# Optimization experiments

Hardware: AMD Instinct MI355X
Metric: run time of the kernel (lower is better)

Reference implementation:

```python
import jax, jax.numpy as jnp
import numpy as np

B = 64          # batch
C = 80          # num_classes
IN_CH = 300     # word-embedding channel
J = 8192        # JOINT_EMB_SIZE (linear_intermediate)
S = 8           # pooling_stride
OUT = J // S    # out_in_tmp = 1024


def setup_inputs() -> dict:
    key = jax.random.key(0)
    ks = jax.random.split(key, 8)
    w = lambda k, sh: jax.random.normal(k, sh, jnp.float32) * 0.02
    return {
        "feature": jax.random.normal(ks[0], (B, 2048, 14, 14), jnp.float32),
        "inp": jax.random.normal(ks[1], (1, C, IN_CH), jnp.float32),
        "A": jax.random.uniform(ks[2], (C, C), jnp.float32),  # positive co-occurrence adjacency
        "W_gc1": w(ks[3], (IN_CH, 1024)),
        "W_gc2": w(ks[4], (1024, 2048)),
        "W_img": w(ks[5], (J, 2048)),
        "b_img": jnp.zeros((J,), jnp.float32),
        "W_cls": w(ks[6], (J, 2048)),
        "b_cls": jnp.zeros((J,), jnp.float32),
        "W_ml": w(ks[7], (C, C * OUT)),
        "b_ml": jnp.zeros((C,), jnp.float32),
    }


def reference(feature, inp, A, W_gc1, W_gc2, W_img, b_img, W_cls, b_cls, W_ml, b_ml):
    # backbone output -> MaxPool2d(14,14) over a 14x14 map == global spatial max
    feat = feature.max(axis=(2, 3))                       # [B, 2048]

    # gen_adj(A).detach(): D = diag(rowsum(A)^-0.5); adj = D @ A.T @ D
    dinv = jnp.sum(A, axis=1) ** -0.5                     # [C]
    adj = jax.lax.stop_gradient(A.T * dinv[:, None] * dinv[None, :])  # [C, C]

    # two GCN layers on label embeddings
    x = adj @ (inp[0] @ W_gc1)                            # [C, 1024]
    x = jax.nn.leaky_relu(x, 0.2)
    x = adj @ (x @ W_gc2)                                 # [C, 2048]

    # MFB bilinear fusion (vectorized form of the nested batch/class loops;
    # dropout is identity in eval mode)
    img = feat @ W_img.T + b_img                          # [B, J]
    cls = x @ W_cls.T + b_cls                             # [C, J]
    # sum-pool over the stride axis of the elementwise product:
    # iq[b,c,o] = sum_s img[b,o*S+s] * cls[c,o*S+s]
    pooled = jnp.einsum('bos,cos->bco',
                        img.reshape(B, OUT, S),
                        cls.reshape(C, OUT, S))           # [B, C, OUT]
    # torch.cat order over class columns -> c-major flatten, then ML_fc_layer
    out = pooled.reshape(B, C * OUT) @ W_ml.T + b_ml      # [B, C]
    return out
```

## Files before the change

kernel.cpp:

```cpp
#include <hip/hip_runtime.h>
#include <hip/hip_bf16.h>
#include <cstdint>
#include <cstddef>

typedef float  f32x4  __attribute__((ext_vector_type(4)));
typedef __bf16 bf16x8 __attribute__((ext_vector_type(8)));
typedef unsigned short u16x8 __attribute__((ext_vector_type(8)));

__device__ __forceinline__ unsigned short f2bf(float f) {
    unsigned u = __float_as_uint(f);
    u += 0x7FFFu + ((u >> 16) & 1u);
    return (unsigned short)(u >> 16);
}


constexpr size_t OFF_FEATB = 0;
constexpr size_t OFF_ADJ   = 262144;
constexpr size_t OFF_Y0    = 287744;
constexpr size_t OFF_X1    = 615424;
constexpr size_t OFF_X2B   = 943104;
constexpr size_t OFF_WG2T  = 1106944;
constexpr size_t OFF_XB    = 9495552;
constexpr size_t OFF_IMG   = 9823232;
constexpr size_t OFF_CLS   = 11920384;
constexpr size_t OFF_G     = 14541824;


__device__ __forceinline__ void maxpool_role(int bid, const float* __restrict__ feature,
                                             unsigned short* __restrict__ featb) {
    int wave = threadIdx.x >> 6, lane = threadIdx.x & 63;
    int r = lane >> 4, q = lane & 15;
    #pragma unroll
    for (int it = 0; it < 4; ++it) {
        int row = bid * 128 + it * 32 + wave * 4 + r;
        const float4* p = (const float4*)(feature + (size_t)row * 196);
        float4 a = p[q], b = p[q + 16], c = p[q + 32];
        float m = fmaxf(fmaxf(fmaxf(a.x, a.y), fmaxf(a.z, a.w)),
                 fmaxf(fmaxf(fmaxf(b.x, b.y), fmaxf(b.z, b.w)),
                       fmaxf(fmaxf(c.x, c.y), fmaxf(c.z, c.w))));
        if (q == 0) {
            float4 d = p[48];
            m = fmaxf(m, fmaxf(fmaxf(d.x, d.y), fmaxf(d.z, d.w)));
        }
        #pragma unroll
        for (int off = 1; off < 16; off <<= 1) m = fmaxf(m, __shfl_xor(m, off));
        if (q == 0) featb[row] = f2bf(m);
    }
}

__device__ __forceinline__ void transpose_role(int idx, const float* __restrict__ in,
                                               float* __restrict__ out, float* t ) {
    int c0 = (idx & 31) * 64, r0 = (idx >> 5) * 64;
    int tx = threadIdx.x & 63, ty = threadIdx.x >> 6;
    #pragma unroll
    for (int i = 0; i < 64; i += 8)
        t[(ty + i) * 65 + tx] = in[(size_t)(r0 + ty + i) * 2048 + c0 + tx];
    __syncthreads();
    #pragma unroll
    for (int i = 0; i < 64; i += 8)
        out[(size_t)(c0 + ty + i) * 1024 + r0 + tx] = t[tx * 65 + (ty + i)];
}

__device__ __forceinline__ void y0_role(int idx, const float* __restrict__ inp,
                                        const float* __restrict__ W1, float* __restrict__ y0) {
    int c = idx >> 1;
    int j = (idx & 1) * 512 + threadIdx.x;
    const float* xr = inp + c * 300;
    float acc = 0.f;
    #pragma unroll 4
    for (int k = 0; k < 300; k++) acc = fmaf(xr[k], W1[k * 1024 + j], acc);
    y0[c * 1024 + j] = acc;
}

__device__ __forceinline__ void adj_role(const float* __restrict__ A, float* __restrict__ adjp,
                                         float* dinv ) {
    int t = threadIdx.x;
    if (t < 80) {
        float s = 0.f;
        for (int j = 0; j < 80; j++) s += A[t * 80 + j];
        dinv[t] = 1.0f / sqrtf(s);
    }
    __syncthreads();
    for (int i = t; i < 6400; i += 512) {
        int r = i / 80, cc = i % 80;
        adjp[i] = A[cc * 80 + r] * dinv[r] * dinv[cc];
    }
}

__device__ __forceinline__ void adjmul_role(int idx, const float* __restrict__ adjp,
                                            const float* __restrict__ xin,
                                            float* __restrict__ outf,
                                            unsigned short* __restrict__ outb, int leaky) {
    int c = idx >> 1;
    int j = (idx & 1) * 512 + threadIdx.x;
    const float* ar = adjp + c * 80;
    float acc = 0.f;
    #pragma unroll 4
    for (int k = 0; k < 80; k++) acc = fmaf(ar[k], xin[k * 1024 + j], acc);
    if (leaky && acc < 0.f) acc *= 0.2f;
    if (outf) outf[c * 1024 + j] = acc;
    if (outb) outb[c * 1024 + j] = f2bf(acc);
}

template <int MF>
__device__ __forceinline__ void gemm_block(int bx, const unsigned short* __restrict__ X,
                                           const float* __restrict__ W,
                                           const float* __restrict__ bias,
                                           float* __restrict__ outf,
                                           unsigned short* __restrict__ outb,
                                           int N, int K, float (*red)[64][21]) {
    int tid = threadIdx.x;
    int wave = tid >> 6, lane = tid & 63;
    int nf = wave & 1, ks = wave >> 1;
    int n = bx * 32 + nf * 16 + (lane & 15);
    int rowa = lane & 15;
    int koff = (lane >> 4) * 8;
    int Kc = K >> 2;
    int k0 = ks * Kc;

    f32x4 acc[MF];
    #pragma unroll
    for (int i = 0; i < MF; i++) acc[i] = (f32x4)(0.f);

    const float* wrow = W + (size_t)n * K;

    #pragma unroll 2
    for (int k = k0; k < k0 + Kc; k += 32) {
        float4 w0 = *(const float4*)(wrow + k + koff);
        float4 w1 = *(const float4*)(wrow + k + koff + 4);
        u16x8 bu;
        bu[0] = f2bf(w0.x); bu[1] = f2bf(w0.y); bu[2] = f2bf(w0.z); bu[3] = f2bf(w0.w);
        bu[4] = f2bf(w1.x); bu[5] = f2bf(w1.y); bu[6] = f2bf(w1.z); bu[7] = f2bf(w1.w);
        bf16x8 bf = __builtin_bit_cast(bf16x8, bu);
        #pragma unroll
        for (int mf = 0; mf < MF; mf++) {
            u16x8 au = *(const u16x8*)(X + (size_t)(mf * 16 + rowa) * K + k + koff);
            acc[mf] = __builtin_amdgcn_mfma_f32_16x16x32_bf16(
                __builtin_bit_cast(bf16x8, au), bf, acc[mf], 0, 0, 0);
        }
    }

    #pragma unroll
    for (int mf = 0; mf < MF; mf++)
        #pragma unroll
        for (int i = 0; i < 4; i++)
            red[wave][lane][mf * 4 + i] = acc[mf][i];
    __syncthreads();

    int lane2 = tid & 63, sg = (tid >> 6) & 3, nf2 = tid >> 8;
    int n2 = bx * 32 + nf2 * 16 + (lane2 & 15);
    float b = bias ? bias[n2] : 0.f;
    #pragma unroll
    for (int mf = 0; mf < MF; mf++) {
        int slot = mf * 4 + sg;
        float s = red[0 + nf2][lane2][slot] + red[2 + nf2][lane2][slot]
                + red[4 + nf2][lane2][slot] + red[6 + nf2][lane2][slot] + b;
        int row = mf * 16 + (lane2 >> 4) * 4 + sg;
        size_t o = (size_t)row * N + n2;
        if (outf) outf[o] = s;
        if (outb) outb[o] = f2bf(s);
    }
}


__global__ __launch_bounds__(512) void k1(const float* __restrict__ feature,
                                          unsigned short* __restrict__ featb,
                                          const float* __restrict__ inp,
                                          const float* __restrict__ W1,
                                          float* __restrict__ y0,
                                          const float* __restrict__ A,
                                          float* __restrict__ adjp,
                                          const float* __restrict__ Wg2,
                                          float* __restrict__ wg2t) {
    __shared__ float lds[64 * 65];
    int b = blockIdx.x;
    if (b < 1024)       maxpool_role(b, feature, featb);
    else if (b < 1536)  transpose_role(b - 1024, Wg2, wg2t, lds);
    else if (b < 1696)  y0_role(b - 1536, inp, W1, y0);
    else                adj_role(A, adjp, lds);
}

__global__ __launch_bounds__(512) void k2(const float* __restrict__ adjp,
                                          const float* __restrict__ y0,
                                          float* __restrict__ x1,
                                          const unsigned short* __restrict__ featb,
                                          const float* __restrict__ W_img,
                                          const float* __restrict__ b_img,
                                          float* __restrict__ img) {
    __shared__ float red[8][64][21];
    int b = blockIdx.x;
    if (b < 160) adjmul_role(b, adjp, y0, x1, nullptr, 1);
    else         gemm_block<4>(b - 160, featb, W_img, b_img, img, nullptr, 8192, 2048, red);
}

__global__ __launch_bounds__(512) void k3(const float* __restrict__ adjp,
                                          const float* __restrict__ x1,
                                          unsigned short* __restrict__ x2b) {
    adjmul_role(blockIdx.x, adjp, x1, nullptr, x2b, 0);
}

__global__ __launch_bounds__(512) void k4(const unsigned short* __restrict__ x2b,
                                          const float* __restrict__ wg2t,
                                          unsigned short* __restrict__ xb) {
    __shared__ float red[8][64][21];
    gemm_block<5>(blockIdx.x, x2b, wg2t, nullptr, nullptr, xb, 2048, 1024, red);
}

__global__ __launch_bounds__(512) void k5(const unsigned short* __restrict__ xb,
                                          const float* __restrict__ W_cls,
                                          const float* __restrict__ b_cls,
                                          float* __restrict__ cls) {
    __shared__ float red[8][64][21];
    gemm_block<5>(blockIdx.x, xb, W_cls, b_cls, cls, nullptr, 8192, 2048, red);
}

__global__ __launch_bounds__(256) void g_kernel(const float* __restrict__ cls,
                                                const float* __restrict__ W_ml,
                                                float* __restrict__ G) {
    __shared__ float wml[16][80][16];
    int c2b = blockIdx.y * 16;
    int o0  = blockIdx.x * 16;
    int j0  = o0 * 8;
    for (int idx = threadIdx.x; idx < 16 * 80 * 16; idx += 256) {
        int ol = idx & 15, c = (idx >> 4) % 80, c2 = idx / 1280;
        wml[c2][c][ol] = W_ml[(size_t)(c2b + c2) * 81920 + c * 1024 + o0 + ol];
    }
    __syncthreads();
    int jl  = threadIdx.x & 127;
    int c2l = (threadIdx.x >> 7) * 8;
    int ol  = jl >> 3;
    float acc[8] = {0.f, 0.f, 0.f, 0.f, 0.f, 0.f, 0.f, 0.f};
    for (int c = 0; c < 80; c++) {
        float cv = cls[(size_t)c * 8192 + j0 + jl];
        #pragma unroll
        for (int i = 0; i < 8; i++) acc[i] = fmaf(cv, wml[c2l + i][c][ol], acc[i]);
    }
    #pragma unroll
    for (int i = 0; i < 8; i++) G[(size_t)(c2b + c2l + i) * 8192 + j0 + jl] = acc[i];
}

__global__ __launch_bounds__(512) void k7(const float* __restrict__ img,
                                          const float* __restrict__ G,
                                          const float* __restrict__ b_ml,
                                          float* __restrict__ out) {
    __shared__ float sm[8][32];
    int btile = blockIdx.x, cg = blockIdx.y;
    int kc = threadIdx.x >> 6, lane = threadIdx.x & 63;
    float acc[4][8];
    #pragma unroll
    for (int q = 0; q < 4; q++)
        #pragma unroll
        for (int i = 0; i < 8; i++) acc[q][i] = 0.f;

    #pragma unroll
    for (int step = 0; step < 4; step++) {
        int k = kc * 1024 + step * 256 + lane * 4;
        float4 gv[8];
        #pragma unroll
        for (int i = 0; i < 8; i++) gv[i] = *(const float4*)(G + (size_t)(cg * 8 + i) * 8192 + k);
        #pragma unroll
        for (int q = 0; q < 4; q++) {
            float4 iv = *(const float4*)(img + (size_t)(btile * 4 + q) * 8192 + k);
            #pragma unroll
            for (int i = 0; i < 8; i++) {
                acc[q][i] = fmaf(iv.x, gv[i].x, acc[q][i]);
                acc[q][i] = fmaf(iv.y, gv[i].y, acc[q][i]);
                acc[q][i] = fmaf(iv.z, gv[i].z, acc[q][i]);
                acc[q][i] = fmaf(iv.w, gv[i].w, acc[q][i]);
            }
        }
    }
    #pragma unroll
    for (int q = 0; q < 4; q++)
        #pragma unroll
        for (int i = 0; i < 8; i++) {
            float v = acc[q][i];
            #pragma unroll
            for (int off = 32; off; off >>= 1) v += __shfl_xor(v, off);
            if (lane == 0) sm[kc][q * 8 + i] = v;
        }
    __syncthreads();
    if (threadIdx.x < 32) {
        int i = threadIdx.x & 7;
        float s = b_ml[cg * 8 + i];
        #pragma unroll
        for (int kk = 0; kk < 8; kk++) s += sm[kk][threadIdx.x];
        int q = threadIdx.x >> 3;
        out[(size_t)(btile * 4 + q) * 80 + cg * 8 + i] = s;
    }
}

extern "C" void kernel_launch(void* const* d_in, const int* in_sizes, int n_in,
                              void* d_out, int out_size, void* d_ws, size_t ws_size,
                              hipStream_t stream) {
    (void)in_sizes; (void)n_in; (void)out_size; (void)ws_size;
    const float* feature = (const float*)d_in[0];
    const float* inp     = (const float*)d_in[1];
    const float* A       = (const float*)d_in[2];
    const float* W_gc1   = (const float*)d_in[3];
    const float* W_gc2   = (const float*)d_in[4];
    const float* W_img   = (const float*)d_in[5];
    const float* b_img   = (const float*)d_in[6];
    const float* W_cls   = (const float*)d_in[7];
    const float* b_cls   = (const float*)d_in[8];
    const float* W_ml    = (const float*)d_in[9];
    const float* b_ml    = (const float*)d_in[10];
    float* out = (float*)d_out;
    char*  ws  = (char*)d_ws;

    unsigned short* featb = (unsigned short*)(ws + OFF_FEATB);
    float* adjp = (float*)(ws + OFF_ADJ);
    float* y0   = (float*)(ws + OFF_Y0);
    float* x1   = (float*)(ws + OFF_X1);
    unsigned short* x2b = (unsigned short*)(ws + OFF_X2B);
    float* wg2t = (float*)(ws + OFF_WG2T);
    unsigned short* xb  = (unsigned short*)(ws + OFF_XB);
    float* img  = (float*)(ws + OFF_IMG);
    float* cls  = (float*)(ws + OFF_CLS);
    float* G    = (float*)(ws + OFF_G);

    k1<<<1697, 512, 0, stream>>>(feature, featb, inp, W_gc1, y0, A, adjp, W_gc2, wg2t);
    k2<<<416,  512, 0, stream>>>(adjp, y0, x1, featb, W_img, b_img, img);
    k3<<<160,  512, 0, stream>>>(adjp, x1, x2b);
    k4<<<64,   512, 0, stream>>>(x2b, wg2t, xb);
    k5<<<256,  512, 0, stream>>>(xb, W_cls, b_cls, cls);
    g_kernel<<<dim3(64, 5), 256, 0, stream>>>(cls, W_ml, G);
    k7<<<dim3(16, 10), 512, 0, stream>>>(img, G, b_ml, out);
}
```

Baseline: 155.8 us.

## Spread maxpool across GCN stages, fuse img GEMM with G kernel, vectorize skinny matmuls

Splits the feature max-pool into four chunks and co-schedules them with the latency-bound GCN kernels (y0, the two adjacency multiplies, and the W_gc2 GEMM). This fills idle compute units during those small stages. The image GEMM moves out of the second kernel and is fused with the G (cls×W_ml) computation in one launch. The skinny matmuls now use float4 loads with a 4-way K split reduced through LDS. The cost is more launch-time role branching and larger shared memory per block in the fused kernel.

```diff
diff --git a/kernel.cpp b/kernel.cpp
--- a/kernel.cpp
+++ b/kernel.cpp
@@ -26,13 +26,14 @@
 constexpr size_t OFF_G     = 14541824;
 
 
-__device__ __forceinline__ void maxpool_role(int bid, const float* __restrict__ feature,
+__device__ __forceinline__ void maxpool_role(int base_row, int bid,
+                                             const float* __restrict__ feature,
                                              unsigned short* __restrict__ featb) {
     int wave = threadIdx.x >> 6, lane = threadIdx.x & 63;
     int r = lane >> 4, q = lane & 15;
     #pragma unroll
     for (int it = 0; it < 4; ++it) {
-        int row = bid * 128 + it * 32 + wave * 4 + r;
+        int row = base_row + bid * 128 + it * 32 + wave * 4 + r;
         const float4* p = (const float4*)(feature + (size_t)row * 196);
         float4 a = p[q], b = p[q + 16], c = p[q + 32];
         float m = fmaxf(fmaxf(fmaxf(a.x, a.y), fmaxf(a.z, a.w)),
@@ -48,6 +49,52 @@
     }
 }
 
+template <int KS>
+__device__ __forceinline__ void skinny_role(int idx, const float* __restrict__ X,
+                                            const float* __restrict__ W,
+                                            float* __restrict__ outf,
+                                            unsigned short* __restrict__ outb,
+                                            int leaky, float4* red ) {
+    int c = idx >> 1, jh = idx & 1;
+    int t = threadIdx.x;
+    int jq = t & 127, ks = t >> 7;
+    int j = jh * 512 + jq * 4;
+    const float* xr = X + c * 4 * KS + ks * KS;
+    const float* wp = W + (size_t)(ks * KS) * 1024 + j;
+    float4 acc = {0.f, 0.f, 0.f, 0.f};
+    #pragma unroll 5
+    for (int k = 0; k < KS; k++) {
+        float a = xr[k];
+        float4 w = *(const float4*)(wp + (size_t)k * 1024);
+        acc.x = fmaf(a, w.x, acc.x);
+        acc.y = fmaf(a, w.y, acc.y);
+        acc.z = fmaf(a, w.z, acc.z);
+        acc.w = fmaf(a, w.w, acc.w);
+    }
+    red[ks * 128 + jq] = acc;
+    __syncthreads();
+    if (ks == 0) {
+        float4 s0 = red[jq], s1 = red[128 + jq], s2 = red[256 + jq], s3 = red[384 + jq];
+        float4 s;
+        s.x = s0.x + s1.x + s2.x + s3.x;
+        s.y = s0.y + s1.y + s2.y + s3.y;
+        s.z = s0.z + s1.z + s2.z + s3.z;
+        s.w = s0.w + s1.w + s2.w + s3.w;
+        if (leaky) {
+            if (s.x < 0.f) s.x *= 0.2f;
+            if (s.y < 0.f) s.y *= 0.2f;
+            if (s.z < 0.f) s.z *= 0.2f;
+            if (s.w < 0.f) s.w *= 0.2f;
+        }
+        size_t o = (size_t)c * 1024 + j;
+        if (outf) *(float4*)(outf + o) = s;
+        if (outb) {
+            unsigned short b4[4] = {f2bf(s.x), f2bf(s.y), f2bf(s.z), f2bf(s.w)};
+            *(uint64_t*)(outb + o) = *(const uint64_t*)b4;
+        }
+    }
+}
+
 __device__ __forceinline__ void transpose_role(int idx, const float* __restrict__ in,
                                                float* __restrict__ out, float* t ) {
     int c0 = (idx & 31) * 64, r0 = (idx >> 5) * 64;
@@ -61,45 +108,24 @@
         out[(size_t)(c0 + ty + i) * 1024 + r0 + tx] = t[tx * 65 + (ty + i)];
 }
 
-__device__ __forceinline__ void y0_role(int idx, const float* __restrict__ inp,
-                                        const float* __restrict__ W1, float* __restrict__ y0) {
-    int c = idx >> 1;
-    int j = (idx & 1) * 512 + threadIdx.x;
-    const float* xr = inp + c * 300;
-    float acc = 0.f;
-    #pragma unroll 4
-    for (int k = 0; k < 300; k++) acc = fmaf(xr[k], W1[k * 1024 + j], acc);
-    y0[c * 1024 + j] = acc;
-}
-
 __device__ __forceinline__ void adj_role(const float* __restrict__ A, float* __restrict__ adjp,
                                          float* dinv ) {
     int t = threadIdx.x;
     if (t < 80) {
-        float s = 0.f;
-        for (int j = 0; j < 80; j++) s += A[t * 80 + j];
-        dinv[t] = 1.0f / sqrtf(s);
+        const float4* ar = (const float4*)(A + t * 80);
+        float4 s4 = {0.f, 0.f, 0.f, 0.f};
+        #pragma unroll
+        for (int j = 0; j < 20; j++) {
+            float4 v = ar[j];
+            s4.x += v.x; s4.y += v.y; s4.z += v.z; s4.w += v.w;
+        }
+        dinv[t] = 1.0f / sqrtf(s4.x + s4.y + s4.z + s4.w);
     }
     __syncthreads();
     for (int i = t; i < 6400; i += 512) {
         int r = i / 80, cc = i % 80;
         adjp[i] = A[cc * 80 + r] * dinv[r] * dinv[cc];
     }
-}
-
-__device__ __forceinline__ void adjmul_role(int idx, const float* __restrict__ adjp,
-                                            const float* __restrict__ xin,
-                                            float* __restrict__ outf,
-                                            unsigned short* __restrict__ outb, int leaky) {
-    int c = idx >> 1;
-    int j = (idx & 1) * 512 + threadIdx.x;
-    const float* ar = adjp + c * 80;
-    float acc = 0.f;
-    #pragma unroll 4
-    for (int k = 0; k < 80; k++) acc = fmaf(ar[k], xin[k * 1024 + j], acc);
-    if (leaky && acc < 0.f) acc *= 0.2f;
-    if (outf) outf[c * 1024 + j] = acc;
-    if (outb) outb[c * 1024 + j] = f2bf(acc);
 }
 
 template <int MF>
@@ -163,86 +189,105 @@
 }
 
 
-__global__ __launch_bounds__(512) void k1(const float* __restrict__ feature,
-                                          unsigned short* __restrict__ featb,
-                                          const float* __restrict__ inp,
-                                          const float* __restrict__ W1,
-                                          float* __restrict__ y0,
-                                          const float* __restrict__ A,
-                                          float* __restrict__ adjp,
-                                          const float* __restrict__ Wg2,
-                                          float* __restrict__ wg2t) {
-    __shared__ float lds[64 * 65];
-    int b = blockIdx.x;
-    if (b < 1024)       maxpool_role(b, feature, featb);
-    else if (b < 1536)  transpose_role(b - 1024, Wg2, wg2t, lds);
-    else if (b < 1696)  y0_role(b - 1536, inp, W1, y0);
-    else                adj_role(A, adjp, lds);
-}
-
-__global__ __launch_bounds__(512) void k2(const float* __restrict__ adjp,
-                                          const float* __restrict__ y0,
-                                          float* __restrict__ x1,
-                                          const unsigned short* __restrict__ featb,
-                                          const float* __restrict__ W_img,
-                                          const float* __restrict__ b_img,
-                                          float* __restrict__ img) {
-    __shared__ float red[8][64][21];
-    int b = blockIdx.x;
-    if (b < 160) adjmul_role(b, adjp, y0, x1, nullptr, 1);
-    else         gemm_block<4>(b - 160, featb, W_img, b_img, img, nullptr, 8192, 2048, red);
-}
-
-__global__ __launch_bounds__(512) void k3(const float* __restrict__ adjp,
-                                          const float* __restrict__ x1,
-                                          unsigned short* __restrict__ x2b) {
-    adjmul_role(blockIdx.x, adjp, x1, nullptr, x2b, 0);
-}
-
-__global__ __launch_bounds__(512) void k4(const unsigned short* __restrict__ x2b,
-                                          const float* __restrict__ wg2t,
-                                          unsigned short* __restrict__ xb) {
-    __shared__ float red[8][64][21];
-    gemm_block<5>(blockIdx.x, x2b, wg2t, nullptr, nullptr, xb, 2048, 1024, red);
-}
-
-__global__ __launch_bounds__(512) void k5(const unsigned short* __restrict__ xb,
-                                          const float* __restrict__ W_cls,
-                                          const float* __restrict__ b_cls,
-                                          float* __restrict__ cls) {
-    __shared__ float red[8][64][21];
+__global__ __launch_bounds__(512, 4) void kA(const float* __restrict__ inp,
+                                             const float* __restrict__ W1,
+                                             float* __restrict__ y0,
+                                             const float* __restrict__ A,
+                                             float* __restrict__ adjp,
+                                             const float* __restrict__ Wg2,
+                                             float* __restrict__ wg2t,
+                                             const float* __restrict__ feature,
+                                             unsigned short* __restrict__ featb) {
+    __shared__ __align__(16) float lds[64 * 65];
+    int b = blockIdx.x;
+    if (b < 160)       skinny_role<75>(b, inp, W1, y0, nullptr, 0, (float4*)lds);
+    else if (b < 161)  adj_role(A, adjp, lds);
+    else if (b < 673)  transpose_role(b - 161, Wg2, wg2t, lds);
+    else               maxpool_role(0, b - 673, feature, featb);
+}
+
+__global__ __launch_bounds__(512, 4) void kB(const float* __restrict__ adjp,
+                                             const float* __restrict__ y0,
+                                             float* __restrict__ x1,
+                                             const float* __restrict__ feature,
+                                             unsigned short* __restrict__ featb) {
+    __shared__ __align__(16) float4 red[512];
+    int b = blockIdx.x;
+    if (b < 160) skinny_role<20>(b, adjp, y0, x1, nullptr, 1, red);
+    else         maxpool_role(32768, b - 160, feature, featb);
+}
+
+__global__ __launch_bounds__(512, 4) void kC(const float* __restrict__ adjp,
+                                             const float* __restrict__ x1,
+                                             unsigned short* __restrict__ x2b,
+                                             const float* __restrict__ feature,
+                                             unsigned short* __restrict__ featb) {
+    __shared__ __align__(16) float4 red[512];
+    int b = blockIdx.x;
+    if (b < 160) skinny_role<20>(b, adjp, x1, nullptr, x2b, 0, red);
+    else         maxpool_role(65536, b - 160, feature, featb);
+}
+
+__global__ __launch_bounds__(512, 4) void kD(const unsigned short* __restrict__ x2b,
+                                             const float* __restrict__ wg2t,
+                                             unsigned short* __restrict__ xb,
+                                             const float* __restrict__ feature,
+                                             unsigned short* __restrict__ featb) {
+    __shared__ __align__(16) float red[8][64][21];
+    int b = blockIdx.x;
+    if (b < 64) gemm_block<5>(b, x2b, wg2t, nullptr, nullptr, xb, 2048, 1024, red);
+    else        maxpool_role(98304, b - 64, feature, featb);
+}
+
+__global__ __launch_bounds__(512, 4) void kE(const unsigned short* __restrict__ xb,
+                                             const float* __restrict__ W_cls,
+                                             const float* __restrict__ b_cls,
+                                             float* __restrict__ cls) {
+    __shared__ __align__(16) float red[8][64][21];
     gemm_block<5>(blockIdx.x, xb, W_cls, b_cls, cls, nullptr, 8192, 2048, red);
 }
 
-__global__ __launch_bounds__(256) void g_kernel(const float* __restrict__ cls,
-                                                const float* __restrict__ W_ml,
-                                                float* __restrict__ G) {
-    __shared__ float wml[16][80][16];
-    int c2b = blockIdx.y * 16;
-    int o0  = blockIdx.x * 16;
-    int j0  = o0 * 8;
-    for (int idx = threadIdx.x; idx < 16 * 80 * 16; idx += 256) {
-        int ol = idx & 15, c = (idx >> 4) % 80, c2 = idx / 1280;
-        wml[c2][c][ol] = W_ml[(size_t)(c2b + c2) * 81920 + c * 1024 + o0 + ol];
-    }
-    __syncthreads();
-    int jl  = threadIdx.x & 127;
-    int c2l = (threadIdx.x >> 7) * 8;
-    int ol  = jl >> 3;
-    float acc[8] = {0.f, 0.f, 0.f, 0.f, 0.f, 0.f, 0.f, 0.f};
-    for (int c = 0; c < 80; c++) {
-        float cv = cls[(size_t)c * 8192 + j0 + jl];
-        #pragma unroll
-        for (int i = 0; i < 8; i++) acc[i] = fmaf(cv, wml[c2l + i][c][ol], acc[i]);
-    }
-    #pragma unroll
-    for (int i = 0; i < 8; i++) G[(size_t)(c2b + c2l + i) * 8192 + j0 + jl] = acc[i];
-}
-
-__global__ __launch_bounds__(512) void k7(const float* __restrict__ img,
-                                          const float* __restrict__ G,
-                                          const float* __restrict__ b_ml,
-                                          float* __restrict__ out) {
+__global__ __launch_bounds__(512, 2) void kF(const unsigned short* __restrict__ featb,
+                                             const float* __restrict__ W_img,
+                                             const float* __restrict__ b_img,
+                                             float* __restrict__ img,
+                                             const float* __restrict__ cls,
+                                             const float* __restrict__ W_ml,
+                                             float* __restrict__ G) {
+    __shared__ __align__(16) float smem[20480];
+    int b = blockIdx.x;
+    if (b < 256) {
+        gemm_block<4>(b, featb, W_img, b_img, img, nullptr, 8192, 2048,
+                      (float (*)[64][21])smem);
+    } else {
+        float (*wml)[80][16] = (float (*)[80][16])smem;
+        int idx = b - 256;
+        int o0 = (idx & 63) * 16;
+        int c2b = (idx >> 6) * 16;
+        int j0 = o0 * 8;
+        for (int i = threadIdx.x; i < 16 * 80 * 16; i += 512) {
+            int ol = i & 15, c = (i >> 4) % 80, c2 = i / 1280;
+            wml[c2][c][ol] = W_ml[(size_t)(c2b + c2) * 81920 + c * 1024 + o0 + ol];
+        }
+        __syncthreads();
+        int jl = threadIdx.x & 127;
+        int c2l = (threadIdx.x >> 7) * 4;
+        int ol = jl >> 3;
+        float acc[4] = {0.f, 0.f, 0.f, 0.f};
+        for (int c = 0; c < 80; c++) {
+            float cv = cls[(size_t)c * 8192 + j0 + jl];
+            #pragma unroll
+            for (int i = 0; i < 4; i++) acc[i] = fmaf(cv, wml[c2l + i][c][ol], acc[i]);
+        }
+        #pragma unroll
+        for (int i = 0; i < 4; i++) G[(size_t)(c2b + c2l + i) * 8192 + j0 + jl] = acc[i];
+    }
+}
+
+__global__ __launch_bounds__(512, 4) void kG(const float* __restrict__ img,
+                                             const float* __restrict__ G,
+                                             const float* __restrict__ b_ml,
+                                             float* __restrict__ out) {
     __shared__ float sm[8][32];
     int btile = blockIdx.x, cg = blockIdx.y;
     int kc = threadIdx.x >> 6, lane = threadIdx.x & 63;
@@ -319,11 +364,11 @@
     float* cls  = (float*)(ws + OFF_CLS);
     float* G    = (float*)(ws + OFF_G);
 
-    k1<<<1697, 512, 0, stream>>>(feature, featb, inp, W_gc1, y0, A, adjp, W_gc2, wg2t);
-    k2<<<416,  512, 0, stream>>>(adjp, y0, x1, featb, W_img, b_img, img);
-    k3<<<160,  512, 0, stream>>>(adjp, x1, x2b);
-    k4<<<64,   512, 0, stream>>>(x2b, wg2t, xb);
-    k5<<<256,  512, 0, stream>>>(xb, W_cls, b_cls, cls);
-    g_kernel<<<dim3(64, 5), 256, 0, stream>>>(cls, W_ml, G);
-    k7<<<dim3(16, 10), 512, 0, stream>>>(img, G, b_ml, out);
-}
+    kA<<<929, 512, 0, stream>>>(inp, W_gc1, y0, A, adjp, W_gc2, wg2t, feature, featb);
+    kB<<<416, 512, 0, stream>>>(adjp, y0, x1, feature, featb);
+    kC<<<416, 512, 0, stream>>>(adjp, x1, x2b, feature, featb);
+    kD<<<320, 512, 0, stream>>>(x2b, wg2t, xb, feature, featb);
+    kE<<<256, 512, 0, stream>>>(xb, W_cls, b_cls, cls);
+    kF<<<576, 512, 0, stream>>>(featb, W_img, b_img, img, cls, W_ml, G);
+    kG<<<dim3(16, 10), 512, 0, stream>>>(img, G, b_ml, out);
+}
```

New measurement: 156.0 us. About the same (+0.1%).
